# Performance work log

Hardware: AMD Instinct MI355X
Metric: run time of the kernel (lower is better)

## Reference

```python
import jax, jax.numpy as jnp
import numpy as np

N_NODES = 50000
X_DIM = 64
EMBED_DIM = 320  # x_dim + hidden*num_hops = 64 + 128*2
N_EDGES = 400000
HIDDEN_MLP = 64
SAMPLE_BIAS = 0.0


def setup_inputs() -> dict:
    key = jax.random.key(0)
    ks = jax.random.split(key, 8)
    x = jax.random.normal(ks[0], (N_NODES, X_DIM), dtype=jnp.float32)
    embed = jax.random.normal(ks[1], (N_NODES, EMBED_DIM), dtype=jnp.float32)
    edge_index = jax.random.randint(ks[2], (2, N_EDGES), 0, N_NODES, dtype=jnp.int64)
    eps = jax.random.uniform(ks[3], (N_EDGES,), dtype=jnp.float32)
    in_channels = 3 * EMBED_DIM
    W1 = jax.random.normal(ks[4], (in_channels, HIDDEN_MLP), dtype=jnp.float32) / np.sqrt(in_channels)
    b1 = jnp.zeros((HIDDEN_MLP,), dtype=jnp.float32)
    W2 = jax.random.normal(ks[5], (HIDDEN_MLP, 1), dtype=jnp.float32) / np.sqrt(HIDDEN_MLP)
    b2 = jnp.zeros((1,), dtype=jnp.float32)
    return {
        'x': x, 'embed': embed, 'edge_index': edge_index, 'node_id': 12345,
        'tmp': jnp.ones((), dtype=jnp.float32), 'eps': eps,
        'W1': W1, 'b1': b1, 'W2': W2, 'b2': b2,
    }


def reference(x, embed, edge_index, node_id, tmp, eps, W1, b1, W2, b2):
    # col, row = edge_index (note: source unpacks col first)
    col = edge_index[0]
    row = edge_index[1]
    E = col.shape[0]
    # gather + concat: [E, 3*embed_dim]
    center = jnp.broadcast_to(embed[node_id][None, :], (E, embed.shape[1]))
    h = jnp.concatenate([embed[col], embed[row], center], axis=-1)
    # 2-layer MLP -> per-edge logit w
    h = jax.nn.relu(h @ W1 + b1)
    w = (h @ W2 + b2).reshape(-1)
    # concrete (Gumbel-sigmoid) relaxation, training=True path
    bias = SAMPLE_BIAS + 0.0001
    e = eps * (1.0 - 2.0 * bias) + bias
    gate = (jnp.log(e) - jnp.log1p(-e) + w) / tmp
    return jax.nn.sigmoid(gate)
```

## Files before the change

### kernel.cpp

```cpp
#include <hip/hip_runtime.h>
#include <math.h>

#define N_NODES   50000
#define EMBED_DIM 320
#define N_EDGES   400000
#define HID       64

typedef __bf16 bf16x8 __attribute__((ext_vector_type(8)));
typedef float  f32x4  __attribute__((ext_vector_type(4)));

__global__ __launch_bounds__(256) void prep_b(const float* __restrict__ W1,
                                              __bf16* __restrict__ Bg) {
    int chunk = blockIdx.x * 256 + threadIdx.x;
    if (chunk >= 5120) return;
    int l  = chunk & 63;
    int sf = chunk >> 6;
    int f  = sf & 7, s = sf >> 3;
    int c  = f * 16 + (l & 15);
    int k0 = s * 32 + (l >> 4) * 8;
    const float* src = W1 + ((size_t)k0 + (c >= 64 ? EMBED_DIM : 0)) * HID + (c & 63);
    __bf16* dst = Bg + (size_t)chunk * 8;
    #pragma unroll
    for (int j = 0; j < 8; ++j) dst[j] = (__bf16)src[(size_t)j * HID];
}

__global__ __launch_bounds__(256) void node_gemm(const float* __restrict__ E,
                                                 const __bf16* __restrict__ Bg,
                                                 const float* __restrict__ W1,
                                                 const float* __restrict__ b1,
                                                 const int* __restrict__ node_id,
                                                 __bf16* __restrict__ P) {
    __shared__ float red[4][64];
    __shared__ float cterm_s[64];
    const int tid = threadIdx.x;

    {
        const int j = tid & 63;
        const int g = tid >> 6;
        const int nid = node_id[0];
        const float* erow = E + (size_t)nid * EMBED_DIM;
        float s = 0.f;
        #pragma unroll 4
        for (int k = g * 80; k < (g + 1) * 80; ++k)
            s = fmaf(erow[k], W1[(size_t)(2 * EMBED_DIM + k) * HID + j], s);
        red[g][j] = s;
    }
    __syncthreads();
    if (tid < 64)
        cterm_s[tid] = b1[tid] + red[0][tid] + red[1][tid] + red[2][tid] + red[3][tid];
    __syncthreads();

    const int wave = tid >> 6;
    const int lane = tid & 63;
    const int r16  = lane & 15;
    const int kg   = lane >> 4;
    const int m0w  = blockIdx.x * 64 + wave * 16;

    int arow_i = m0w + r16;
    if (arow_i > N_NODES - 1) arow_i = N_NODES - 1;
    const float*  arow  = E + (size_t)arow_i * EMBED_DIM + kg * 8;
    const __bf16* bbase = Bg + (size_t)lane * 8;

    f32x4 acc[8] = {};

    float4 aA[10][2];
    #pragma unroll
    for (int s = 0; s < 10; ++s) {
        aA[s][0] = *(const float4*)(arow + s * 32 + 0);
        aA[s][1] = *(const float4*)(arow + s * 32 + 4);
    }

    bf16x8 bB[2][8];
    #pragma unroll
    for (int f = 0; f < 8; ++f)
        bB[0][f] = *(const bf16x8*)(bbase + (size_t)f * 512);

    #pragma unroll
    for (int s = 0; s < 10; ++s) {
        const int cur = s & 1, nxt = cur ^ 1;
        if (s < 9) {
            #pragma unroll
            for (int f = 0; f < 8; ++f)
                bB[nxt][f] = *(const bf16x8*)(bbase + (size_t)((s + 1) * 8 + f) * 512);
        }
        bf16x8 av;
        av[0] = (__bf16)aA[s][0].x; av[1] = (__bf16)aA[s][0].y;
        av[2] = (__bf16)aA[s][0].z; av[3] = (__bf16)aA[s][0].w;
        av[4] = (__bf16)aA[s][1].x; av[5] = (__bf16)aA[s][1].y;
        av[6] = (__bf16)aA[s][1].z; av[7] = (__bf16)aA[s][1].w;
        #pragma unroll
        for (int f = 0; f < 8; ++f)
            acc[f] = __builtin_amdgcn_mfma_f32_16x16x32_bf16(av, bB[cur][f], acc[f], 0, 0, 0);
    }

    #pragma unroll
    for (int f = 0; f < 8; ++f) {
        float ct = (f < 4) ? cterm_s[f * 16 + r16] : 0.f;
        #pragma unroll
        for (int j = 0; j < 4; ++j) {
            int gr = m0w + kg * 4 + j;
            if (gr < N_NODES)
                P[(size_t)gr * 128 + f * 16 + r16] = (__bf16)(acc[f][j] + ct);
        }
    }
}

__global__ __launch_bounds__(256) void edge_kernel(const int* __restrict__ eidx,
                                                   const float* __restrict__ eps,
                                                   const __bf16* __restrict__ P,
                                                   const float* __restrict__ W2,
                                                   const float* __restrict__ b2,
                                                   const float* __restrict__ tmp,
                                                   float* __restrict__ out) {
    const int gid = blockIdx.x * blockDim.x + threadIdx.x;
    const int e   = gid >> 3;
    const int q   = gid & 7;
    if (e >= N_EDGES) return;

    int col = eidx[e];
    int row = eidx[N_EDGES + e];
    col = min(max(col, 0), N_NODES - 1);
    row = min(max(row, 0), N_NODES - 1);

    bf16x8 a = *(const bf16x8*)(P + (size_t)col * 128 + q * 8);
    bf16x8 c = *(const bf16x8*)(P + (size_t)row * 128 + 64 + q * 8);
    float4 w0 = *(const float4*)(W2 + q * 8);
    float4 w1 = *(const float4*)(W2 + q * 8 + 4);

    float s = 0.f;
    s = fmaf(fmaxf((float)a[0] + (float)c[0], 0.f), w0.x, s);
    s = fmaf(fmaxf((float)a[1] + (float)c[1], 0.f), w0.y, s);
    s = fmaf(fmaxf((float)a[2] + (float)c[2], 0.f), w0.z, s);
    s = fmaf(fmaxf((float)a[3] + (float)c[3], 0.f), w0.w, s);
    s = fmaf(fmaxf((float)a[4] + (float)c[4], 0.f), w1.x, s);
    s = fmaf(fmaxf((float)a[5] + (float)c[5], 0.f), w1.y, s);
    s = fmaf(fmaxf((float)a[6] + (float)c[6], 0.f), w1.z, s);
    s = fmaf(fmaxf((float)a[7] + (float)c[7], 0.f), w1.w, s);

    s += __shfl_xor(s, 1);
    s += __shfl_xor(s, 2);
    s += __shfl_xor(s, 4);

    if (q == 0) {
        float w  = s + b2[0];
        const float bias = 0.0001f;
        float ee = eps[e] * (1.0f - 2.0f * bias) + bias;
        float gate = (logf(ee) - log1pf(-ee) + w) / tmp[0];
        out[e] = 1.0f / (1.0f + expf(-gate));
    }
}

extern "C" void kernel_launch(void* const* d_in, const int* in_sizes, int n_in,
                              void* d_out, int out_size, void* d_ws, size_t ws_size,
                              hipStream_t stream) {
    const float* embed = (const float*)d_in[1];
    const int*   eidx  = (const int*)d_in[2];
    const int*   nid   = (const int*)d_in[3];
    const float* tmp   = (const float*)d_in[4];
    const float* eps   = (const float*)d_in[5];
    const float* W1    = (const float*)d_in[6];
    const float* b1    = (const float*)d_in[7];
    const float* W2    = (const float*)d_in[8];
    const float* b2    = (const float*)d_in[9];
    float*       out   = (float*)d_out;

    __bf16* P  = (__bf16*)d_ws;
    __bf16* Bg = (__bf16*)((char*)d_ws + (size_t)N_NODES * 128 * sizeof(__bf16));

    prep_b<<<20, 256, 0, stream>>>(W1, Bg);

    int gemm_blocks = (N_NODES + 63) / 64;
    node_gemm<<<gemm_blocks, 256, 0, stream>>>(embed, Bg, W1, b1, nid, P);

    int edge_threads = N_EDGES * 8;
    edge_kernel<<<(edge_threads + 255) / 256, 256, 0, stream>>>(
        eidx, eps, P, W2, b2, tmp, out);
}
```

Measured before the change: 162.6 us.

## Stage embed tile in LDS via async copies and hoist center-term precompute

Moves the center-node term computation out of every node_gemm block into one extra block of the prep kernel, which writes it to global workspace. node_gemm now loads its 64x320 fp32 A tile into LDS with global_load_lds async copies using an XOR swizzle, then reads A fragments from LDS. B fragments are prefetched four stages deep instead of two. This removes redundant per-block center dot products and uses coalesced async loads, at the cost of 80KB of LDS per block, which limits occupancy.

```diff
diff --git a/kernel.cpp b/kernel.cpp
--- a/kernel.cpp
+++ b/kernel.cpp
@@ -1,5 +1,6 @@
 #include <hip/hip_runtime.h>
 #include <math.h>
+#include <stdint.h>
 
 #define N_NODES   50000
 #define EMBED_DIM 320
@@ -9,32 +10,33 @@
 typedef __bf16 bf16x8 __attribute__((ext_vector_type(8)));
 typedef float  f32x4  __attribute__((ext_vector_type(4)));
 
+__device__ __forceinline__ void async_copy16(void* lds_dst, const void* g_src) {
+    __builtin_amdgcn_global_load_lds(
+        (const __attribute__((address_space(1))) uint32_t*)g_src,
+        (__attribute__((address_space(3))) uint32_t*)lds_dst,
+        16, 0, 0);
+}
+
 __global__ __launch_bounds__(256) void prep_b(const float* __restrict__ W1,
-                                              __bf16* __restrict__ Bg) {
-    int chunk = blockIdx.x * 256 + threadIdx.x;
-    if (chunk >= 5120) return;
-    int l  = chunk & 63;
-    int sf = chunk >> 6;
-    int f  = sf & 7, s = sf >> 3;
-    int c  = f * 16 + (l & 15);
-    int k0 = s * 32 + (l >> 4) * 8;
-    const float* src = W1 + ((size_t)k0 + (c >= 64 ? EMBED_DIM : 0)) * HID + (c & 63);
-    __bf16* dst = Bg + (size_t)chunk * 8;
-    #pragma unroll
-    for (int j = 0; j < 8; ++j) dst[j] = (__bf16)src[(size_t)j * HID];
-}
-
-__global__ __launch_bounds__(256) void node_gemm(const float* __restrict__ E,
-                                                 const __bf16* __restrict__ Bg,
-                                                 const float* __restrict__ W1,
-                                                 const float* __restrict__ b1,
-                                                 const int* __restrict__ node_id,
-                                                 __bf16* __restrict__ P) {
-    __shared__ float red[4][64];
-    __shared__ float cterm_s[64];
-    const int tid = threadIdx.x;
-
-    {
+                                              const float* __restrict__ b1,
+                                              const int* __restrict__ node_id,
+                                              const float* __restrict__ E,
+                                              __bf16* __restrict__ Bg,
+                                              float* __restrict__ cterm_g) {
+    if (blockIdx.x < 20) {
+        int chunk = blockIdx.x * 256 + threadIdx.x;
+        int l  = chunk & 63;
+        int sf = chunk >> 6;
+        int f  = sf & 7, s = sf >> 3;
+        int c  = f * 16 + (l & 15);
+        int k0 = s * 32 + (l >> 4) * 8;
+        const float* src = W1 + ((size_t)k0 + (c >= 64 ? EMBED_DIM : 0)) * HID + (c & 63);
+        __bf16* dst = Bg + (size_t)chunk * 8;
+        #pragma unroll
+        for (int j = 0; j < 8; ++j) dst[j] = (__bf16)src[(size_t)j * HID];
+    } else {
+        __shared__ float red[4][64];
+        const int tid = threadIdx.x;
         const int j = tid & 63;
         const int g = tid >> 6;
         const int nid = node_id[0];
@@ -44,63 +46,87 @@
         for (int k = g * 80; k < (g + 1) * 80; ++k)
             s = fmaf(erow[k], W1[(size_t)(2 * EMBED_DIM + k) * HID + j], s);
         red[g][j] = s;
-    }
-    __syncthreads();
-    if (tid < 64)
-        cterm_s[tid] = b1[tid] + red[0][tid] + red[1][tid] + red[2][tid] + red[3][tid];
-    __syncthreads();
-
+        __syncthreads();
+        if (tid < 64)
+            cterm_g[tid] = b1[tid] + red[0][tid] + red[1][tid] + red[2][tid] + red[3][tid];
+    }
+}
+
+__global__ __launch_bounds__(256) void node_gemm(const float* __restrict__ E,
+                                                 const __bf16* __restrict__ Bg,
+                                                 const float* __restrict__ cterm_g,
+                                                 __bf16* __restrict__ P) {
+    __shared__ float sA[64 * EMBED_DIM];
+
+    const int tid  = threadIdx.x;
     const int wave = tid >> 6;
     const int lane = tid & 63;
     const int r16  = lane & 15;
     const int kg   = lane >> 4;
-    const int m0w  = blockIdx.x * 64 + wave * 16;
-
-    int arow_i = m0w + r16;
-    if (arow_i > N_NODES - 1) arow_i = N_NODES - 1;
-    const float*  arow  = E + (size_t)arow_i * EMBED_DIM + kg * 8;
+    const int m0   = blockIdx.x * 64;
+
+    #pragma unroll
+    for (int it = 0; it < 20; ++it) {
+        int g   = it * 256 + tid;
+        int r   = g / 80;
+        int cw  = g - r * 80;
+        int scw = cw ^ (r & 7);
+        int gr  = m0 + r;
+        if (gr > N_NODES - 1) gr = N_NODES - 1;
+        async_copy16((char*)sA + (size_t)g * 16,
+                     E + (size_t)gr * EMBED_DIM + scw * 4);
+    }
+
+    float ct[4];
+    #pragma unroll
+    for (int f = 0; f < 4; ++f) ct[f] = cterm_g[f * 16 + r16];
+
     const __bf16* bbase = Bg + (size_t)lane * 8;
+    bf16x8 bB[4][8];
+    #pragma unroll
+    for (int s = 0; s < 4; ++s)
+        #pragma unroll
+        for (int f = 0; f < 8; ++f)
+            bB[s][f] = *(const bf16x8*)(bbase + (size_t)(s * 8 + f) * 512);
 
     f32x4 acc[8] = {};
 
-    float4 aA[10][2];
+    asm volatile("s_waitcnt vmcnt(0)" ::: "memory");
+    __syncthreads();
+
+    const int rt      = wave * 16 + r16;
+    const int rowbase = rt * EMBED_DIM;
     #pragma unroll
     for (int s = 0; s < 10; ++s) {
-        aA[s][0] = *(const float4*)(arow + s * 32 + 0);
-        aA[s][1] = *(const float4*)(arow + s * 32 + 4);
-    }
-
-    bf16x8 bB[2][8];
-    #pragma unroll
-    for (int f = 0; f < 8; ++f)
-        bB[0][f] = *(const bf16x8*)(bbase + (size_t)f * 512);
-
-    #pragma unroll
-    for (int s = 0; s < 10; ++s) {
-        const int cur = s & 1, nxt = cur ^ 1;
-        if (s < 9) {
+        int cb = s * 8 + kg * 2;
+        int c0 = cb ^ (r16 & 7);
+        int c1 = (cb + 1) ^ (r16 & 7);
+        f32x4 lo = *(const f32x4*)&sA[rowbase + c0 * 4];
+        f32x4 hi = *(const f32x4*)&sA[rowbase + c1 * 4];
+        bf16x8 av;
+        av[0] = (__bf16)lo[0]; av[1] = (__bf16)lo[1];
+        av[2] = (__bf16)lo[2]; av[3] = (__bf16)lo[3];
+        av[4] = (__bf16)hi[0]; av[5] = (__bf16)hi[1];
+        av[6] = (__bf16)hi[2]; av[7] = (__bf16)hi[3];
+        #pragma unroll
+        for (int f = 0; f < 8; ++f)
+            acc[f] = __builtin_amdgcn_mfma_f32_16x16x32_bf16(av, bB[s & 3][f], acc[f], 0, 0, 0);
+        if (s < 6) {
             #pragma unroll
             for (int f = 0; f < 8; ++f)
-                bB[nxt][f] = *(const bf16x8*)(bbase + (size_t)((s + 1) * 8 + f) * 512);
+                bB[s & 3][f] = *(const bf16x8*)(bbase + (size_t)((s + 4) * 8 + f) * 512);
         }
-        bf16x8 av;
-        av[0] = (__bf16)aA[s][0].x; av[1] = (__bf16)aA[s][0].y;
-        av[2] = (__bf16)aA[s][0].z; av[3] = (__bf16)aA[s][0].w;
-        av[4] = (__bf16)aA[s][1].x; av[5] = (__bf16)aA[s][1].y;
-        av[6] = (__bf16)aA[s][1].z; av[7] = (__bf16)aA[s][1].w;
-        #pragma unroll
-        for (int f = 0; f < 8; ++f)
-            acc[f] = __builtin_amdgcn_mfma_f32_16x16x32_bf16(av, bB[cur][f], acc[f], 0, 0, 0);
-    }
-
+    }
+
+    const int m0w = m0 + wave * 16;
     #pragma unroll
     for (int f = 0; f < 8; ++f) {
-        float ct = (f < 4) ? cterm_s[f * 16 + r16] : 0.f;
+        float c = (f < 4) ? ct[f] : 0.f;
         #pragma unroll
         for (int j = 0; j < 4; ++j) {
             int gr = m0w + kg * 4 + j;
             if (gr < N_NODES)
-                P[(size_t)gr * 128 + f * 16 + r16] = (__bf16)(acc[f][j] + ct);
+                P[(size_t)gr * 128 + f * 16 + r16] = (__bf16)(acc[f][j] + c);
         }
     }
 }
@@ -164,13 +190,14 @@
     const float* b2    = (const float*)d_in[9];
     float*       out   = (float*)d_out;
 
-    __bf16* P  = (__bf16*)d_ws;
-    __bf16* Bg = (__bf16*)((char*)d_ws + (size_t)N_NODES * 128 * sizeof(__bf16));
-
-    prep_b<<<20, 256, 0, stream>>>(W1, Bg);
+    __bf16* P       = (__bf16*)d_ws;
+    __bf16* Bg      = (__bf16*)((char*)d_ws + (size_t)N_NODES * 128 * sizeof(__bf16));
+    float*  cterm_g = (float*)((char*)Bg + (size_t)5120 * 8 * sizeof(__bf16));
+
+    prep_b<<<21, 256, 0, stream>>>(W1, b1, nid, embed, Bg, cterm_g);
 
     int gemm_blocks = (N_NODES + 63) / 64;
-    node_gemm<<<gemm_blocks, 256, 0, stream>>>(embed, Bg, W1, b1, nid, P);
+    node_gemm<<<gemm_blocks, 256, 0, stream>>>(embed, Bg, cterm_g, P);
 
     int edge_threads = N_EDGES * 8;
     edge_kernel<<<(edge_threads + 255) / 256, 256, 0, stream>>>(
```

After: 148.3 us. 1.1x faster.
